# Performance work log

Hardware: AMD Instinct MI355X
Metric: run time of the kernel (lower is better)

The kernel has to match this reference:

```python
import jax, jax.numpy as jnp
import numpy as np

B, T, I, H, L = 128, 512, 512, 1024, 2
KEEP = 0.9  # 1 - dropout_rate


def setup_inputs() -> dict:
    key = jax.random.key(0)
    ks = jax.random.split(key, 13)
    s = 0.02
    bern = lambda k, shape: (jax.random.bernoulli(k, KEEP, shape) / KEEP).astype(jnp.float32)
    return {
        "x": jax.random.normal(ks[0], (B, T, I), dtype=jnp.float32),
        "W_ih0": jax.random.normal(ks[1], (4 * H, I), dtype=jnp.float32) * s,
        "W_hh0": jax.random.normal(ks[2], (4 * H, H), dtype=jnp.float32) * s,
        "b_ih0": jax.random.normal(ks[3], (4 * H,), dtype=jnp.float32) * s,
        "b_hh0": jax.random.normal(ks[4], (4 * H,), dtype=jnp.float32) * s,
        "W_ih1": jax.random.normal(ks[5], (4 * H, H), dtype=jnp.float32) * s,
        "W_hh1": jax.random.normal(ks[6], (4 * H, H), dtype=jnp.float32) * s,
        "b_ih1": jax.random.normal(ks[7], (4 * H,), dtype=jnp.float32) * s,
        "b_hh1": jax.random.normal(ks[8], (4 * H,), dtype=jnp.float32) * s,
        "out_mask": bern(ks[9], (L, B, H)),
        "h_mask": bern(ks[10], (L, B, H)),
        "c_mask": bern(ks[11], (L, B, H)),
    }


def _run_layer(x_tbi, W_ih, W_hh, b_ih, b_hh, om, hm, cm):
    """x_tbi: [T,B,in]; masks: [B,H]. Returns ([T,B,H] outputs, final (h,c))."""
    h0 = jnp.zeros((x_tbi.shape[1], H), dtype=x_tbi.dtype)
    c0 = jnp.zeros_like(h0)
    # precompute input projections for all timesteps: [T,B,4H]
    xg = jnp.einsum('tbi,gi->tbg', x_tbi, W_ih) + b_ih + b_hh

    def step(carry, xg_t):
        h, c = carry
        gates = xg_t + h @ W_hh.T  # [B,4H]
        i, f, g, o = jnp.split(gates, 4, axis=-1)
        i, f, o = jax.nn.sigmoid(i), jax.nn.sigmoid(f), jax.nn.sigmoid(o)
        g = jnp.tanh(g)
        c2 = f * c + i * g
        h2 = o * jnp.tanh(c2)
        out = h2 * om
        return (h2 * hm, c2 * cm), out

    (hf, cf), ys = jax.lax.scan(step, (h0, c0), xg)
    return ys, (hf, cf)


def reference(x, W_ih0, W_hh0, b_ih0, b_hh0, W_ih1, W_hh1, b_ih1, b_hh1,
              out_mask, h_mask, c_mask):
    layers = [(W_ih0, W_hh0, b_ih0, b_hh0), (W_ih1, W_hh1, b_ih1, b_hh1)]
    xt = jnp.transpose(x, (1, 0, 2))  # [T,B,I]
    for l, (Wi, Wh, bi, bh) in enumerate(layers):
        xt, (hf, cf) = _run_layer(xt, Wi, Wh, bi, bh,
                                  out_mask[l], h_mask[l], c_mask[l])
    out = jnp.transpose(xt, (1, 0, 2))  # [B,T,H]
    return out, (hf[None], cf[None])
```

## Files before the change

### kernel.cpp

```cpp
#include <hip/hip_runtime.h>

#define B_  128
#define T_  512
#define I_  512
#define H_  1024
#define G4  4096
#define SLOT 262144L
#define SENTW 0xFFFFFFFFu

typedef __attribute__((ext_vector_type(8))) short   short8;
typedef __attribute__((ext_vector_type(4))) short   short4v;
typedef __attribute__((ext_vector_type(4))) float   f32x4;
typedef __attribute__((ext_vector_type(4))) int     int4v;
typedef unsigned long long u64;

__device__ __forceinline__ float bf2f(short u){
  return __uint_as_float(((unsigned)(unsigned short)u) << 16);
}
__device__ __forceinline__ short f2bf(float f){
  unsigned u = __float_as_uint(f);
  unsigned r = (u + 0x7FFFu + ((u >> 16) & 1u)) >> 16;
  return (short)r;
}
__device__ __forceinline__ float sigm(float x){ return 1.0f/(1.0f + __expf(-x)); }
__device__ __forceinline__ float tanh_(float x){ return 1.0f - 2.0f/(__expf(2.0f*x) + 1.0f); }
__device__ __forceinline__ bool okq(u64 a){
  return ((unsigned)a != SENTW) & ((unsigned)(a >> 32) != SENTW);
}
__device__ __forceinline__ int okv(int4v c){
  return (c.x != -1) & (c.y != -1) & (c.z != -1) & (c.w != -1);
}
__device__ __forceinline__ void ldst16(const short* g, short* lp){
  __builtin_amdgcn_global_load_lds(
      (const __attribute__((address_space(1))) void*)g,
      (__attribute__((address_space(3))) void*)lp, 16, 0, 0);
}

__global__ __launch_bounds__(256) void cvt_bf16(const float* __restrict__ in,
                                                short* __restrict__ out, int nq){
  int i = blockIdx.x*256 + threadIdx.x;
  if (i >= nq) return;
  float4 v = ((const float4*)in)[i];
  short4v o; o.x = f2bf(v.x); o.y = f2bf(v.y); o.z = f2bf(v.z); o.w = f2bf(v.w);
  ((short4v*)out)[i] = o;
}

__global__ __launch_bounds__(256) void swz_whh(const float* __restrict__ W,
                                               short* __restrict__ out){
  int c = blockIdx.x*256 + threadIdx.x;
  int l = c & 63, ks = (c >> 6) & 15, ct = (c >> 10) & 1, wvv = (c >> 11) & 7, jb = c >> 14;
  int g = wvv >> 1, kh = wvv & 1;
  long row = (long)(g*1024 + jb*32 + ct*16 + (l & 15));
  int col = kh*512 + ks*32 + (l >> 4)*8;
  const float* src = W + row*H_ + col;
  short8 o;
#pragma unroll
  for (int e = 0; e < 8; ++e) o[e] = f2bf(src[e]);
  ((short8*)out)[c] = o;
}

template<int K>
__global__ __launch_bounds__(256) void proj_gemm(const short* __restrict__ A,
                                                 const short* __restrict__ W,
                                                 const float* __restrict__ bih,
                                                 const float* __restrict__ bhh,
                                                 short* __restrict__ C){
  __shared__ __align__(16) short sh[16896];
  const int tid = threadIdx.x;
  const int l  = tid & 63, wv = tid >> 6;
  const int wm = wv >> 1,  wn = wv & 1;
  const int nt = blockIdx.x, mt = blockIdx.y;
  const int NK = K/32;

  const int srow = wv*32 + (l >> 2);
  const int scol = (l & 3)*8;
  const short* Ag = A + (long)(mt*128 + srow)*K + scol;
  const short* Wg = W + (long)(nt*128 + srow)*K + scol;

  auto stage = [&](int buf, int kt){
#pragma unroll
    for (int j = 0; j < 2; ++j){
      short* la = &sh[buf*8192 +        (wv*32 + j*16)*32];
      short* lb = &sh[buf*8192 + 4096 + (wv*32 + j*16)*32];
      ldst16(Ag + (long)(j*16)*K + kt*32, la);
      ldst16(Wg + (long)(j*16)*K + kt*32, lb);
    }
  };

  stage(0, 0);

  f32x4 acc[4][4];
  f32x4 z = {0.f,0.f,0.f,0.f};
#pragma unroll
  for (int i = 0; i < 4; ++i)
#pragma unroll
    for (int j = 0; j < 4; ++j) acc[i][j] = z;

  for (int kt = 0; kt < NK; ++kt){
    __syncthreads();
    if (kt + 1 < NK) stage((kt + 1) & 1, kt + 1);
    const short* As = &sh[(kt & 1)*8192];
    const short* Bs = &sh[(kt & 1)*8192 + 4096];
    short8 bfr[4];
#pragma unroll
    for (int nf = 0; nf < 4; ++nf)
      bfr[nf] = *(const short8*)&Bs[(wn*64 + nf*16 + (l & 15))*32 + (l >> 4)*8];
#pragma unroll
    for (int mf = 0; mf < 4; ++mf){
      short8 af = *(const short8*)&As[(wm*64 + mf*16 + (l & 15))*32 + (l >> 4)*8];
#pragma unroll
      for (int nf = 0; nf < 4; ++nf)
        acc[mf][nf] = __builtin_amdgcn_mfma_f32_16x16x32_bf16(af, bfr[nf], acc[mf][nf], 0, 0, 0);
    }
  }

  __syncthreads();
  short* cst = sh;
#pragma unroll
  for (int nf = 0; nf < 4; ++nf){
    int nc = wn*64 + nf*16 + (l & 15);
    int n  = nt*128 + nc;
    float bs = bih[n] + bhh[n];
#pragma unroll
    for (int mf = 0; mf < 4; ++mf){
#pragma unroll
      for (int r = 0; r < 4; ++r){
        int mr = wm*64 + mf*16 + (l >> 4)*4 + r;
        cst[mr*132 + nc] = f2bf(acc[mf][nf][r] + bs);
      }
    }
  }
  __syncthreads();
  const long m0 = (long)mt*128;
  const int  n0 = nt*128;
#pragma unroll
  for (int i = 0; i < 8; ++i){
    int sid = i*256 + tid;
    int mr = sid >> 4, seg = sid & 15;
    *(short8*)&C[(m0 + mr)*G4 + n0 + seg*8] = *(const short8*)&cst[mr*132 + seg*8];
  }
}

template<int LAYER, bool RING>
__global__ __launch_bounds__(512, 2) void lstm_scan(
    short* __restrict__ hring,
    const short* __restrict__ Wsw, const short* __restrict__ xg,
    const float* __restrict__ om, const float* __restrict__ hm, const float* __restrict__ cm,
    short* __restrict__ out0, float* __restrict__ dout,
    int* __restrict__ flags)
{
  const int tid = threadIdx.x;
  const int l = tid & 63, wv = tid >> 6;
  const int bt = blockIdx.x, jb = blockIdx.y;

  short8 w0[16], w1[16];
  {
    const short8* wp = (const short8*)Wsw + ((long)((jb*8 + wv)*2)*16)*64 + l;
#pragma unroll
    for (int ks = 0; ks < 16; ++ks) w0[ks] = wp[ks*64];
#pragma unroll
    for (int ks = 0; ks < 16; ++ks) w1[ks] = wp[(16 + ks)*64];
    f32x4* wf0 = (f32x4*)w0;
    f32x4* wf1 = (f32x4*)w1;
#pragma unroll
    for (int i = 0; i < 16; ++i){ asm volatile("" : "+v"(wf0[i])); asm volatile("" : "+v"(wf1[i])); }
  }

  const int idx = wv*8 + (l >> 3);
  const int bl  = idx & 15;
  const int jl  = ((idx >> 4) << 3) + (l & 7);
  const int jcol = jb*32 + jl;
  const long bj = (long)(bt*16 + bl)*H_ + jcol;
  const float mo = om[bj], mh = hm[bj], mc = cm[bj];
  float c = 0.f;
  const int ct_r = jl >> 4;
  const int lane_src = (jl & 15) + ((bl >> 2) << 4);
  const int rr = bl & 3;
  const int kh = wv & 1;

  __shared__ __align__(16) short hbuf[2048*8];
  __shared__ float red[16*264];
  __shared__ __align__(16) short sstage[512];
  int* flbase = flags + (long)bt*T_*32;

  const int ch0 = wv*256 +   0 + l;
  const int ch1 = wv*256 +  64 + l;
  const int ch2 = wv*256 + 128 + l;
  const int ch3 = wv*256 + 192 + l;

  const long xbase = (long)(bt*16 + bl)*T_*G4 + jcol;
  short xv0 = xg[xbase], xv1 = xg[xbase + H_], xv2 = xg[xbase + 2*H_], xv3 = xg[xbase + 3*H_];

  for (int t = 0; t < T_; ++t){
    const long slotoff  = RING ? (long)t*SLOT     : (long)(t & 1)*SLOT;
    const long nslotoff = RING ? (long)(t+1)*SLOT : (long)((t+1) & 1)*SLOT;

    if (t > 0){
      const char* hb = (const char*)hring + slotoff + (long)bt*32768;
      if constexpr (RING){
        int4v c0 = *(const int4v*)(hb + (long)ch0*16);
        int4v c1 = *(const int4v*)(hb + (long)ch1*16);
        int4v c2 = *(const int4v*)(hb + (long)ch2*16);
        int4v c3 = *(const int4v*)(hb + (long)ch3*16);
        int ok = 0;
        if (okv(c0)){ *(int4v*)&hbuf[ch0*8] = c0; ok |= 1; }
        if (okv(c1)){ *(int4v*)&hbuf[ch1*8] = c1; ok |= 2; }
        if (okv(c2)){ *(int4v*)&hbuf[ch2*8] = c2; ok |= 4; }
        if (okv(c3)){ *(int4v*)&hbuf[ch3*8] = c3; ok |= 8; }
        if (ok != 15){
          const u64* hp = (const u64*)hb;
          int spins = 0;
          while (true){
            if (!(ok & 1)){
              u64 a = __hip_atomic_load(hp + (long)ch0*2,     __ATOMIC_RELAXED, __HIP_MEMORY_SCOPE_AGENT);
              u64 b = __hip_atomic_load(hp + (long)ch0*2 + 1, __ATOMIC_RELAXED, __HIP_MEMORY_SCOPE_AGENT);
              if (okq(a) & okq(b)){ u64* d = (u64*)&hbuf[ch0*8]; d[0] = a; d[1] = b; ok |= 1; }
            }
            if (!(ok & 2)){
              u64 a = __hip_atomic_load(hp + (long)ch1*2,     __ATOMIC_RELAXED, __HIP_MEMORY_SCOPE_AGENT);
              u64 b = __hip_atomic_load(hp + (long)ch1*2 + 1, __ATOMIC_RELAXED, __HIP_MEMORY_SCOPE_AGENT);
              if (okq(a) & okq(b)){ u64* d = (u64*)&hbuf[ch1*8]; d[0] = a; d[1] = b; ok |= 2; }
            }
            if (!(ok & 4)){
              u64 a = __hip_atomic_load(hp + (long)ch2*2,     __ATOMIC_RELAXED, __HIP_MEMORY_SCOPE_AGENT);
              u64 b = __hip_atomic_load(hp + (long)ch2*2 + 1, __ATOMIC_RELAXED, __HIP_MEMORY_SCOPE_AGENT);
              if (okq(a) & okq(b)){ u64* d = (u64*)&hbuf[ch2*8]; d[0] = a; d[1] = b; ok |= 4; }
            }
            if (!(ok & 8)){
              u64 a = __hip_atomic_load(hp + (long)ch3*2,     __ATOMIC_RELAXED, __HIP_MEMORY_SCOPE_AGENT);
              u64 b = __hip_atomic_load(hp + (long)ch3*2 + 1, __ATOMIC_RELAXED, __HIP_MEMORY_SCOPE_AGENT);
              if (okq(a) & okq(b)){ u64* d = (u64*)&hbuf[ch3*8]; d[0] = a; d[1] = b; ok |= 8; }
            }
            if (ok == 15) break;
            if (++spins > (1 << 20)) break;
            if (spins > 2) __builtin_amdgcn_s_sleep(2);
          }
        }
      } else {
        const u64* hp = (const u64*)hb;
        short8 vv[4];
#pragma unroll
        for (int i = 0; i < 4; ++i){
          const u64* ap = hp + (long)(wv*256 + i*64 + l)*2;
          union { u64 q[2]; short8 s; } uu;
          uu.q[0] = __hip_atomic_load(ap,     __ATOMIC_RELAXED, __HIP_MEMORY_SCOPE_AGENT);
          uu.q[1] = __hip_atomic_load(ap + 1, __ATOMIC_RELAXED, __HIP_MEMORY_SCOPE_AGENT);
          vv[i] = uu.s;
        }
#pragma unroll
        for (int i = 0; i < 4; ++i)
          *(short8*)&hbuf[(wv*256 + i*64 + l)*8] = vv[i];
      }
      __syncthreads();

      f32x4 a00 = {0.f,0.f,0.f,0.f}, a01 = {0.f,0.f,0.f,0.f};
      f32x4 a10 = {0.f,0.f,0.f,0.f}, a11 = {0.f,0.f,0.f,0.f};
#pragma unroll
      for (int ks = 0; ks < 16; ++ks){
        short8 av = *(const short8*)&hbuf[((kh*16 + ks)*64 + l)*8];
        if (ks & 1){
          a01 = __builtin_amdgcn_mfma_f32_16x16x32_bf16(av, w0[ks], a01, 0, 0, 0);
          a11 = __builtin_amdgcn_mfma_f32_16x16x32_bf16(av, w1[ks], a11, 0, 0, 0);
        } else {
          a00 = __builtin_amdgcn_mfma_f32_16x16x32_bf16(av, w0[ks], a00, 0, 0, 0);
          a10 = __builtin_amdgcn_mfma_f32_16x16x32_bf16(av, w1[ks], a10, 0, 0, 0);
        }
      }
      f32x4 s0, s1;
#pragma unroll
      for (int r = 0; r < 4; ++r){ s0[r] = a00[r] + a01[r]; s1[r] = a10[r] + a11[r]; }
      *(f32x4*)&red[(wv*2 + 0)*264 + l*4] = s0;
      *(f32x4*)&red[(wv*2 + 1)*264 + l*4] = s1;
      __syncthreads();
    }

    float gate[4];
    short xvv[4] = {xv0, xv1, xv2, xv3};
#pragma unroll
    for (int g = 0; g < 4; ++g){
      float rv = 0.f;
      if (t > 0){
        rv = red[((g*2 + 0)*2 + ct_r)*264 + lane_src*4 + rr]
           + red[((g*2 + 1)*2 + ct_r)*264 + lane_src*4 + rr];
      }
      gate[g] = rv + bf2f(xvv[g]);
    }
    float ii = sigm(gate[0]);
    float ff = sigm(gate[1]);
    float gg = tanh_(gate[2]);
    float oo = sigm(gate[3]);
    float c2 = ff*c + ii*gg;
    float h2 = oo*tanh_(c2);
    c = c2*mc;
    float hn = h2*mh;

    if (t == T_ - 1){
      if (LAYER == 0){
        out0[((long)(bt*16 + bl)*T_ + t)*H_ + jcol] = f2bf(h2*mo);
      } else {
        dout[((long)(bt*16 + bl)*T_ + t)*H_ + jcol] = h2*mo;
        dout[(long)B_*T_*H_ + bj] = hn;
        dout[(long)B_*T_*H_ + (long)B_*H_ + bj] = c;
      }
      break;
    }

    sstage[wv*64 + l] = f2bf(hn);
    asm volatile("s_waitcnt lgkmcnt(0)" ::: "memory");
    __builtin_amdgcn_sched_barrier(0);
    if (l < 8){
      short8 pk = *(const short8*)&sstage[wv*64 + l*8];
      char* hdst = (char*)hring + nslotoff
                 + ((long)bt*2048 + jb*64 + wv*8 + l)*16;
      if constexpr (RING){
        asm volatile("global_store_dwordx4 %0, %1, off sc1" :: "v"(hdst), "v"(pk) : "memory");
      } else {
        union { short8 s; u64 q[2]; } uu; uu.s = pk;
        u64* qp = (u64*)hdst;
        __hip_atomic_store(qp,     uu.q[0], __ATOMIC_RELAXED, __HIP_MEMORY_SCOPE_AGENT);
        __hip_atomic_store(qp + 1, uu.q[1], __ATOMIC_RELAXED, __HIP_MEMORY_SCOPE_AGENT);
      }
    }
    if constexpr (!RING){
      asm volatile("s_waitcnt vmcnt(0)" ::: "memory");
      __syncthreads();
      if (tid == 0)
        __hip_atomic_store(&flbase[(long)t*32 + jb], 1,
                           __ATOMIC_RELAXED, __HIP_MEMORY_SCOPE_AGENT);
    }

    if (LAYER == 0){
      out0[((long)(bt*16 + bl)*T_ + t)*H_ + jcol] = f2bf(h2*mo);
    } else {
      dout[((long)(bt*16 + bl)*T_ + t)*H_ + jcol] = h2*mo;
    }
    {
      const short* xp = xg + xbase + (long)(t + 1)*G4;
      xv0 = xp[0]; xv1 = xp[H_]; xv2 = xp[2*H_]; xv3 = xp[3*H_];
    }

    if constexpr (!RING){
      const u64* fp = (const u64*)&flbase[(long)t*32];
      int spins = 0;
      while (true){
        int ok = 1;
        if (l < 16){
          u64 v = __hip_atomic_load(fp + l, __ATOMIC_RELAXED, __HIP_MEMORY_SCOPE_AGENT);
          ok = ((unsigned)v != 0u) & ((unsigned)(v >> 32) != 0u);
        }
        if (__all(ok)) break;
        if (++spins > (1 << 20)) break;
        if (spins > 8) __builtin_amdgcn_s_sleep(1);
      }
      __builtin_amdgcn_sched_barrier(0);
      __builtin_amdgcn_fence(__ATOMIC_ACQUIRE, "workgroup");
    }
  }
}

extern "C" void kernel_launch(void* const* d_in, const int* in_sizes, int n_in,
                              void* d_out, int out_size, void* d_ws, size_t ws_size,
                              hipStream_t stream){
  const float* x    = (const float*)d_in[0];
  const float* Wih0 = (const float*)d_in[1];
  const float* Whh0 = (const float*)d_in[2];
  const float* bih0 = (const float*)d_in[3];
  const float* bhh0 = (const float*)d_in[4];
  const float* Wih1 = (const float*)d_in[5];
  const float* Whh1 = (const float*)d_in[6];
  const float* bih1 = (const float*)d_in[7];
  const float* bhh1 = (const float*)d_in[8];
  const float* omsk = (const float*)d_in[9];
  const float* hmsk = (const float*)d_in[10];
  const float* cmsk = (const float*)d_in[11];
  float* out = (float*)d_out;

  char* p = (char*)d_ws;
  auto alloc = [&](size_t bytes)->char*{
    char* r = p; p += (bytes + 255) & ~(size_t)255; return r;
  };
  short* xg      = (short*)alloc((size_t)65536*4096*2);
  short* out0_bf = (short*)alloc((size_t)67108864*2);
  short* x_bf    = (short*)out0_bf;
  short* wih0_bf = (short*)alloc((size_t)2097152*2);
  short* wih1_bf = (short*)alloc((size_t)4194304*2);
  short* whh0_sw = (short*)alloc((size_t)4194304*2);
  short* whh1_sw = (short*)alloc((size_t)4194304*2);
  int*   flags0  = (int*)alloc((size_t)8*512*32*4);
  int*   flags1  = (int*)alloc((size_t)8*512*32*4);
  size_t fixed = (size_t)(p - (char*)d_ws);
  bool ring = (fixed + (size_t)512*SLOT) <= ws_size;
  size_t ringbytes = ring ? (size_t)512*SLOT : (size_t)2*SLOT;
  short* hring = (short*)alloc(ringbytes);
  if ((size_t)(p - (char*)d_ws) > ws_size) return;

  if (!ring){
    hipMemsetAsync(flags0, 0, (size_t)8*512*32*4, stream);
    hipMemsetAsync(flags1, 0, (size_t)8*512*32*4, stream);
  }
  hipMemsetAsync(hring, 0xFF, ringbytes, stream);

  cvt_bf16<<<33554432/4/256, 256, 0, stream>>>(x,    x_bf,    33554432/4);
  cvt_bf16<<<2097152/4/256,  256, 0, stream>>>(Wih0, wih0_bf, 2097152/4);
  cvt_bf16<<<4194304/4/256,  256, 0, stream>>>(Wih1, wih1_bf, 4194304/4);
  swz_whh <<<524288/256,     256, 0, stream>>>(Whh0, whh0_sw);
  swz_whh <<<524288/256,     256, 0, stream>>>(Whh1, whh1_sw);

  proj_gemm<512><<<dim3(32, 512), 256, 0, stream>>>(x_bf, wih0_bf, bih0, bhh0, xg);
  if (ring)
    lstm_scan<0, true ><<<dim3(8, 32), 512, 0, stream>>>(hring, whh0_sw, xg,
        omsk, hmsk, cmsk, out0_bf, nullptr, flags0);
  else
    lstm_scan<0, false><<<dim3(8, 32), 512, 0, stream>>>(hring, whh0_sw, xg,
        omsk, hmsk, cmsk, out0_bf, nullptr, flags0);

  hipMemsetAsync(hring, 0xFF, ringbytes, stream);

  proj_gemm<1024><<<dim3(32, 512), 256, 0, stream>>>(out0_bf, wih1_bf, bih1, bhh1, xg);
  if (ring)
    lstm_scan<1, true ><<<dim3(8, 32), 512, 0, stream>>>(hring, whh1_sw, xg,
        omsk + 131072, hmsk + 131072, cmsk + 131072, nullptr, out, flags1);
  else
    lstm_scan<1, false><<<dim3(8, 32), 512, 0, stream>>>(hring, whh1_sw, xg,
        omsk + 131072, hmsk + 131072, cmsk + 131072, nullptr, out, flags1);
}
```

Before: 3.822 ms.

## Fuse layer-1 input projection GEMM into layer-0 scan kernel with spin-wait overlap

The layer-1 input-projection GEMM moves into the layer-0 recurrent scan kernel as 8192 extra workgroups. These tiles poll the layer-0 output buffer, which is pre-filled with a sentinel by a new memset, until their rows are written, then compute and store the layer-1 gate projections into xg. The goal is to hide the separate projection GEMM launch behind the latency-bound sequential scan. In exchange there is an extra 128 MB memset, GEMM blocks that spin and compete with scan blocks for memory and CUs, and a reliance on low-index scan blocks being dispatched and resident first. xg is overwritten while layer 0 may still be reading later timesteps.

```diff
diff --git a/kernel.cpp b/kernel.cpp
--- a/kernel.cpp
+++ b/kernel.cpp
@@ -141,12 +141,329 @@
   }
 }
 
-template<int LAYER, bool RING>
-__global__ __launch_bounds__(512, 2) void lstm_scan(
+template<bool RING>
+__global__ __launch_bounds__(512, 2) void fused1(
+    short* __restrict__ hring,
+    const short* __restrict__ Wsw, short* __restrict__ xg,
+    const float* __restrict__ om, const float* __restrict__ hm, const float* __restrict__ cm,
+    short* __restrict__ out0,
+    const short* __restrict__ Wih1,
+    const float* __restrict__ bih1, const float* __restrict__ bhh1,
+    int* __restrict__ flags)
+{
+  __shared__ __align__(16) char smem[50688];
+  const int tid = threadIdx.x;
+  const int l = tid & 63, wv = tid >> 6;
+
+  if (blockIdx.x < 256){
+    const int bt = blockIdx.x & 7, jb = blockIdx.x >> 3;
+    short* hbuf = (short*)smem;
+    float* red  = (float*)(smem + 32768);
+    short* sstage = (short*)(smem + 49664);
+
+    short8 w0[16], w1[16];
+    {
+      const short8* wp = (const short8*)Wsw + ((long)((jb*8 + wv)*2)*16)*64 + l;
+#pragma unroll
+      for (int ks = 0; ks < 16; ++ks) w0[ks] = wp[ks*64];
+#pragma unroll
+      for (int ks = 0; ks < 16; ++ks) w1[ks] = wp[(16 + ks)*64];
+      f32x4* wf0 = (f32x4*)w0;
+      f32x4* wf1 = (f32x4*)w1;
+#pragma unroll
+      for (int i = 0; i < 16; ++i){ asm volatile("" : "+v"(wf0[i])); asm volatile("" : "+v"(wf1[i])); }
+    }
+
+    const int idx = wv*8 + (l >> 3);
+    const int bl  = idx & 15;
+    const int jl  = ((idx >> 4) << 3) + (l & 7);
+    const int jcol = jb*32 + jl;
+    const long bj = (long)(bt*16 + bl)*H_ + jcol;
+    const float mo = om[bj], mh = hm[bj], mc = cm[bj];
+    float c = 0.f;
+    const int ct_r = jl >> 4;
+    const int lane_src = (jl & 15) + ((bl >> 2) << 4);
+    const int rr = bl & 3;
+    const int kh = wv & 1;
+    int* flbase = flags + (long)bt*T_*32;
+
+    const int ch0 = wv*256 +   0 + l;
+    const int ch1 = wv*256 +  64 + l;
+    const int ch2 = wv*256 + 128 + l;
+    const int ch3 = wv*256 + 192 + l;
+
+    const long xbase = (long)(bt*16 + bl)*T_*G4 + jcol;
+    short xv0 = xg[xbase], xv1 = xg[xbase + H_], xv2 = xg[xbase + 2*H_], xv3 = xg[xbase + 3*H_];
+
+    for (int t = 0; t < T_; ++t){
+      const long slotoff  = RING ? (long)t*SLOT     : (long)(t & 1)*SLOT;
+      const long nslotoff = RING ? (long)(t+1)*SLOT : (long)((t+1) & 1)*SLOT;
+
+      if (t > 0){
+        const char* hb = (const char*)hring + slotoff + (long)bt*32768;
+        if constexpr (RING){
+          int4v c0 = *(const int4v*)(hb + (long)ch0*16);
+          int4v c1 = *(const int4v*)(hb + (long)ch1*16);
+          int4v c2 = *(const int4v*)(hb + (long)ch2*16);
+          int4v c3 = *(const int4v*)(hb + (long)ch3*16);
+          int ok = 0;
+          if (okv(c0)){ *(int4v*)&hbuf[ch0*8] = c0; ok |= 1; }
+          if (okv(c1)){ *(int4v*)&hbuf[ch1*8] = c1; ok |= 2; }
+          if (okv(c2)){ *(int4v*)&hbuf[ch2*8] = c2; ok |= 4; }
+          if (okv(c3)){ *(int4v*)&hbuf[ch3*8] = c3; ok |= 8; }
+          if (ok != 15){
+            const u64* hp = (const u64*)hb;
+            int spins = 0;
+            while (true){
+              if (!(ok & 1)){
+                u64 a = __hip_atomic_load(hp + (long)ch0*2,     __ATOMIC_RELAXED, __HIP_MEMORY_SCOPE_AGENT);
+                u64 b = __hip_atomic_load(hp + (long)ch0*2 + 1, __ATOMIC_RELAXED, __HIP_MEMORY_SCOPE_AGENT);
+                if (okq(a) & okq(b)){ u64* d = (u64*)&hbuf[ch0*8]; d[0] = a; d[1] = b; ok |= 1; }
+              }
+              if (!(ok & 2)){
+                u64 a = __hip_atomic_load(hp + (long)ch1*2,     __ATOMIC_RELAXED, __HIP_MEMORY_SCOPE_AGENT);
+                u64 b = __hip_atomic_load(hp + (long)ch1*2 + 1, __ATOMIC_RELAXED, __HIP_MEMORY_SCOPE_AGENT);
+                if (okq(a) & okq(b)){ u64* d = (u64*)&hbuf[ch1*8]; d[0] = a; d[1] = b; ok |= 2; }
+              }
+              if (!(ok & 4)){
+                u64 a = __hip_atomic_load(hp + (long)ch2*2,     __ATOMIC_RELAXED, __HIP_MEMORY_SCOPE_AGENT);
+                u64 b = __hip_atomic_load(hp + (long)ch2*2 + 1, __ATOMIC_RELAXED, __HIP_MEMORY_SCOPE_AGENT);
+                if (okq(a) & okq(b)){ u64* d = (u64*)&hbuf[ch2*8]; d[0] = a; d[1] = b; ok |= 4; }
+              }
+              if (!(ok & 8)){
+                u64 a = __hip_atomic_load(hp + (long)ch3*2,     __ATOMIC_RELAXED, __HIP_MEMORY_SCOPE_AGENT);
+                u64 b = __hip_atomic_load(hp + (long)ch3*2 + 1, __ATOMIC_RELAXED, __HIP_MEMORY_SCOPE_AGENT);
+                if (okq(a) & okq(b)){ u64* d = (u64*)&hbuf[ch3*8]; d[0] = a; d[1] = b; ok |= 8; }
+              }
+              if (ok == 15) break;
+              if (++spins > (1 << 20)) break;
+              if (spins > 2) __builtin_amdgcn_s_sleep(2);
+            }
+          }
+        } else {
+          const u64* hp = (const u64*)hb;
+          short8 vv[4];
+#pragma unroll
+          for (int i = 0; i < 4; ++i){
+            const u64* ap = hp + (long)(wv*256 + i*64 + l)*2;
+            union { u64 q[2]; short8 s; } uu;
+            uu.q[0] = __hip_atomic_load(ap,     __ATOMIC_RELAXED, __HIP_MEMORY_SCOPE_AGENT);
+            uu.q[1] = __hip_atomic_load(ap + 1, __ATOMIC_RELAXED, __HIP_MEMORY_SCOPE_AGENT);
+            vv[i] = uu.s;
+          }
+#pragma unroll
+          for (int i = 0; i < 4; ++i)
+            *(short8*)&hbuf[(wv*256 + i*64 + l)*8] = vv[i];
+        }
+        __syncthreads();
+
+        f32x4 a00 = {0.f,0.f,0.f,0.f}, a01 = {0.f,0.f,0.f,0.f};
+        f32x4 a10 = {0.f,0.f,0.f,0.f}, a11 = {0.f,0.f,0.f,0.f};
+#pragma unroll
+        for (int ks = 0; ks < 16; ++ks){
+          short8 av = *(const short8*)&hbuf[((kh*16 + ks)*64 + l)*8];
+          if (ks & 1){
+            a01 = __builtin_amdgcn_mfma_f32_16x16x32_bf16(av, w0[ks], a01, 0, 0, 0);
+            a11 = __builtin_amdgcn_mfma_f32_16x16x32_bf16(av, w1[ks], a11, 0, 0, 0);
+          } else {
+            a00 = __builtin_amdgcn_mfma_f32_16x16x32_bf16(av, w0[ks], a00, 0, 0, 0);
+            a10 = __builtin_amdgcn_mfma_f32_16x16x32_bf16(av, w1[ks], a10, 0, 0, 0);
+          }
+        }
+        f32x4 s0, s1;
+#pragma unroll
+        for (int r = 0; r < 4; ++r){ s0[r] = a00[r] + a01[r]; s1[r] = a10[r] + a11[r]; }
+        *(f32x4*)&red[(wv*2 + 0)*264 + l*4] = s0;
+        *(f32x4*)&red[(wv*2 + 1)*264 + l*4] = s1;
+        __syncthreads();
+      }
+
+      float gate[4];
+      short xvv[4] = {xv0, xv1, xv2, xv3};
+#pragma unroll
+      for (int g = 0; g < 4; ++g){
+        float rv = 0.f;
+        if (t > 0){
+          rv = red[((g*2 + 0)*2 + ct_r)*264 + lane_src*4 + rr]
+             + red[((g*2 + 1)*2 + ct_r)*264 + lane_src*4 + rr];
+        }
+        gate[g] = rv + bf2f(xvv[g]);
+      }
+      float ii = sigm(gate[0]);
+      float ff = sigm(gate[1]);
+      float gg = tanh_(gate[2]);
+      float oo = sigm(gate[3]);
+      float c2 = ff*c + ii*gg;
+      float h2 = oo*tanh_(c2);
+      c = c2*mc;
+      float hn = h2*mh;
+
+      {
+        short* op = out0 + ((long)(bt*16 + bl)*T_ + t)*H_ + jcol;
+        int ov = (unsigned short)f2bf(h2*mo);
+        asm volatile("global_store_short %0, %1, off sc1" :: "v"(op), "v"(ov) : "memory");
+      }
+
+      if (t == T_ - 1) break;
+
+      sstage[wv*64 + l] = f2bf(hn);
+      asm volatile("s_waitcnt lgkmcnt(0)" ::: "memory");
+      __builtin_amdgcn_sched_barrier(0);
+      if (l < 8){
+        short8 pk = *(const short8*)&sstage[wv*64 + l*8];
+        char* hdst = (char*)hring + nslotoff
+                   + ((long)bt*2048 + jb*64 + wv*8 + l)*16;
+        if constexpr (RING){
+          asm volatile("global_store_dwordx4 %0, %1, off sc1" :: "v"(hdst), "v"(pk) : "memory");
+        } else {
+          union { short8 s; u64 q[2]; } uu; uu.s = pk;
+          u64* qp = (u64*)hdst;
+          __hip_atomic_store(qp,     uu.q[0], __ATOMIC_RELAXED, __HIP_MEMORY_SCOPE_AGENT);
+          __hip_atomic_store(qp + 1, uu.q[1], __ATOMIC_RELAXED, __HIP_MEMORY_SCOPE_AGENT);
+        }
+      }
+      if constexpr (!RING){
+        asm volatile("s_waitcnt vmcnt(0)" ::: "memory");
+        __syncthreads();
+        if (tid == 0)
+          __hip_atomic_store(&flbase[(long)t*32 + jb], 1,
+                             __ATOMIC_RELAXED, __HIP_MEMORY_SCOPE_AGENT);
+      }
+
+      {
+        const short* xp = xg + xbase + (long)(t + 1)*G4;
+        xv0 = xp[0]; xv1 = xp[H_]; xv2 = xp[2*H_]; xv3 = xp[3*H_];
+      }
+
+      if constexpr (!RING){
+        const u64* fp = (const u64*)&flbase[(long)t*32];
+        int spins = 0;
+        while (true){
+          int ok = 1;
+          if (l < 16){
+            u64 v = __hip_atomic_load(fp + l, __ATOMIC_RELAXED, __HIP_MEMORY_SCOPE_AGENT);
+            ok = ((unsigned)v != 0u) & ((unsigned)(v >> 32) != 0u);
+          }
+          if (__all(ok)) break;
+          if (++spins > (1 << 20)) break;
+          if (spins > 8) __builtin_amdgcn_s_sleep(1);
+        }
+        __builtin_amdgcn_sched_barrier(0);
+        __builtin_amdgcn_fence(__ATOMIC_ACQUIRE, "workgroup");
+      }
+    }
+  } else {
+    const int p = (int)blockIdx.x - 256;
+    const int trange = p >> 11;
+    const int bidx   = (p >> 4) & 127;
+    const int ntl    = p & 15;
+    const int mt = bidx*4 + trange;
+    const long m0 = (long)mt*128;
+    const int  n0 = ntl*256;
+
+    short* sm = (short*)smem;
+    const int wm = wv >> 2, wn = wv & 3;
+
+    const int rA  = tid >> 2;
+    const int ccA = (tid & 3)*8;
+    const short* Asrc = out0 + (m0 + rA)*1024 + ccA;
+    const short* Wg = Wih1 + (long)(n0 + wv*32 + (l >> 2))*1024 + (l & 3)*8;
+
+    auto ldA = [&](int kt, int4v &va){
+      const char* pa = (const char*)(Asrc + kt*32);
+      va = *(const int4v*)pa;
+      if (!okv(va)){
+        const u64* ap = (const u64*)pa;
+        int spins = 0;
+        while (true){
+          u64 a = __hip_atomic_load(ap,     __ATOMIC_RELAXED, __HIP_MEMORY_SCOPE_AGENT);
+          u64 b = __hip_atomic_load(ap + 1, __ATOMIC_RELAXED, __HIP_MEMORY_SCOPE_AGENT);
+          if (okq(a) & okq(b)){
+            union { u64 q[2]; int4v v; } u; u.q[0] = a; u.q[1] = b; va = u.v; break;
+          }
+          if (++spins > (1 << 20)) break;
+          if (spins > 1) __builtin_amdgcn_s_sleep(8);
+        }
+      }
+    };
+    auto stB = [&](int buf, int kt){
+#pragma unroll
+      for (int j = 0; j < 2; ++j)
+        ldst16(Wg + (long)(j*16)*1024 + kt*32, sm + buf*12288 + 4096 + (wv*32 + j*16)*32);
+    };
+
+    int4v av;
+    ldA(0, av);
+    stB(0, 0);
+    *(int4v*)&sm[0*12288 + rA*32 + ccA] = av;
+
+    f32x4 acc[4][4];
+    f32x4 z = {0.f,0.f,0.f,0.f};
+#pragma unroll
+    for (int i = 0; i < 4; ++i)
+#pragma unroll
+      for (int j = 0; j < 4; ++j) acc[i][j] = z;
+
+    for (int kt = 0; kt < 32; ++kt){
+      __syncthreads();
+      int4v nv;
+      if (kt + 1 < 32){ stB((kt + 1) & 1, kt + 1); ldA(kt + 1, nv); }
+      const short* As = sm + (kt & 1)*12288;
+      const short* Bs = As + 4096;
+      short8 bfr[4];
+#pragma unroll
+      for (int nf = 0; nf < 4; ++nf)
+        bfr[nf] = *(const short8*)&Bs[(wn*64 + nf*16 + (l & 15))*32 + (l >> 4)*8];
+#pragma unroll
+      for (int mf = 0; mf < 4; ++mf){
+        short8 af = *(const short8*)&As[(wm*64 + mf*16 + (l & 15))*32 + (l >> 4)*8];
+#pragma unroll
+        for (int nf = 0; nf < 4; ++nf)
+          acc[mf][nf] = __builtin_amdgcn_mfma_f32_16x16x32_bf16(af, bfr[nf], acc[mf][nf], 0, 0, 0);
+      }
+      if (kt + 1 < 32)
+        *(int4v*)&sm[((kt + 1) & 1)*12288 + rA*32 + ccA] = nv;
+    }
+
+    __syncthreads();
+    short* cst = sm;
+#pragma unroll
+    for (int hh = 0; hh < 2; ++hh){
+      if ((wn >> 1) == hh){
+#pragma unroll
+        for (int nf = 0; nf < 4; ++nf){
+          int ncol = wn*64 + nf*16 + (l & 15);
+          int n = n0 + ncol;
+          float bs = bih1[n] + bhh1[n];
+          int lcol = ncol - hh*128;
+#pragma unroll
+          for (int mf = 0; mf < 4; ++mf){
+#pragma unroll
+            for (int r4 = 0; r4 < 4; ++r4){
+              int mr = wm*64 + mf*16 + (l >> 4)*4 + r4;
+              cst[mr*132 + lcol] = f2bf(acc[mf][nf][r4] + bs);
+            }
+          }
+        }
+      }
+      __syncthreads();
+#pragma unroll
+      for (int i = 0; i < 4; ++i){
+        int sid = i*512 + tid;
+        int mr = sid >> 4, seg = sid & 15;
+        *(short8*)&xg[(m0 + mr)*G4 + n0 + hh*128 + seg*8] = *(const short8*)&cst[mr*132 + seg*8];
+      }
+      __syncthreads();
+    }
+  }
+}
+
+template<bool RING>
+__global__ __launch_bounds__(512, 2) void lstm_scan1(
     short* __restrict__ hring,
     const short* __restrict__ Wsw, const short* __restrict__ xg,
     const float* __restrict__ om, const float* __restrict__ hm, const float* __restrict__ cm,
-    short* __restrict__ out0, float* __restrict__ dout,
+    float* __restrict__ dout,
     int* __restrict__ flags)
 {
   const int tid = threadIdx.x;
@@ -295,13 +612,9 @@
     float hn = h2*mh;
 
     if (t == T_ - 1){
-      if (LAYER == 0){
-        out0[((long)(bt*16 + bl)*T_ + t)*H_ + jcol] = f2bf(h2*mo);
-      } else {
-        dout[((long)(bt*16 + bl)*T_ + t)*H_ + jcol] = h2*mo;
-        dout[(long)B_*T_*H_ + bj] = hn;
-        dout[(long)B_*T_*H_ + (long)B_*H_ + bj] = c;
-      }
+      dout[((long)(bt*16 + bl)*T_ + t)*H_ + jcol] = h2*mo;
+      dout[(long)B_*T_*H_ + bj] = hn;
+      dout[(long)B_*T_*H_ + (long)B_*H_ + bj] = c;
       break;
     }
 
@@ -329,11 +642,7 @@
                            __ATOMIC_RELAXED, __HIP_MEMORY_SCOPE_AGENT);
     }
 
-    if (LAYER == 0){
-      out0[((long)(bt*16 + bl)*T_ + t)*H_ + jcol] = f2bf(h2*mo);
-    } else {
-      dout[((long)(bt*16 + bl)*T_ + t)*H_ + jcol] = h2*mo;
-    }
+    dout[((long)(bt*16 + bl)*T_ + t)*H_ + jcol] = h2*mo;
     {
       const short* xp = xg + xbase + (long)(t + 1)*G4;
       xv0 = xp[0]; xv1 = xp[H_]; xv2 = xp[2*H_]; xv3 = xp[3*H_];
@@ -407,20 +716,22 @@
   swz_whh <<<524288/256,     256, 0, stream>>>(Whh1, whh1_sw);
 
   proj_gemm<512><<<dim3(32, 512), 256, 0, stream>>>(x_bf, wih0_bf, bih0, bhh0, xg);
+
+  hipMemsetAsync(out0_bf, 0xFF, (size_t)67108864*2, stream);
+
   if (ring)
-    lstm_scan<0, true ><<<dim3(8, 32), 512, 0, stream>>>(hring, whh0_sw, xg,
-        omsk, hmsk, cmsk, out0_bf, nullptr, flags0);
+    fused1<true ><<<dim3(256 + 8192), 512, 0, stream>>>(hring, whh0_sw, xg,
+        omsk, hmsk, cmsk, out0_bf, wih1_bf, bih1, bhh1, flags0);
   else
-    lstm_scan<0, false><<<dim3(8, 32), 512, 0, stream>>>(hring, whh0_sw, xg,
-        omsk, hmsk, cmsk, out0_bf, nullptr, flags0);
+    fused1<false><<<dim3(256 + 8192), 512, 0, stream>>>(hring, whh0_sw, xg,
+        omsk, hmsk, cmsk, out0_bf, wih1_bf, bih1, bhh1, flags0);
 
   hipMemsetAsync(hring, 0xFF, ringbytes, stream);
 
-  proj_gemm<1024><<<dim3(32, 512), 256, 0, stream>>>(out0_bf, wih1_bf, bih1, bhh1, xg);
   if (ring)
-    lstm_scan<1, true ><<<dim3(8, 32), 512, 0, stream>>>(hring, whh1_sw, xg,
-        omsk + 131072, hmsk + 131072, cmsk + 131072, nullptr, out, flags1);
+    lstm_scan1<true ><<<dim3(8, 32), 512, 0, stream>>>(hring, whh1_sw, xg,
+        omsk + 131072, hmsk + 131072, cmsk + 131072, out, flags1);
   else
-    lstm_scan<1, false><<<dim3(8, 32), 512, 0, stream>>>(hring, whh1_sw, xg,
-        omsk + 131072, hmsk + 131072, cmsk + 131072, nullptr, out, flags1);
-}
+    lstm_scan1<false><<<dim3(8, 32), 512, 0, stream>>>(hring, whh1_sw, xg,
+        omsk + 131072, hmsk + 131072, cmsk + 131072, out, flags1);
+}
```

Result: slower. 5.209 ms (+36.3%).
